# Kernel tuning notes

Measured on AMD Instinct MI355X. Metric: run time of the kernel, lower is better.

Reference implementation:

```python
import jax, jax.numpy as jnp
import numpy as np


def setup_inputs() -> dict:
    key = jax.random.key(0)
    kq, kv, ks = jax.random.split(key, 3)
    B, T, nh, N, D = 4, 2048, 8, 64, 128
    Q = jax.random.normal(kq, (B, T, nh, N), dtype=jnp.float32)
    V = jax.random.normal(kv, (B, T, D), dtype=jnp.float32)
    state = jax.random.normal(ks, (B, nh, N, D), dtype=jnp.float32)
    return {"Q": Q, "V": V, "state": state, "return_new_state": 1}


def reference(Q, V, state, return_new_state):
    # Inter-chunk: read recurrent state.  Q:[B,T,nh,N] x state:[B,nh,N,D] -> [B,T,nh,D]
    output = jnp.einsum('BTnN,BnND->BTnD', Q, state)
    new_state = None
    if return_new_state:
        # Q.flatten(2).mT @ V, unflattened: outer-product accumulation Q^T V
        new_state = state + jnp.einsum('BTnN,BTD->BnND', Q, V)
    T = Q.shape[1]
    if T > 1:
        # Strictly-causal intra-chunk term: tril(QQ^T, -1) @ V
        scores = jnp.tril(jnp.einsum('BTnN,BUnN->BnTU', Q, Q), k=-1)
        output = output + jnp.einsum('BnTU,BUD->BTnD', scores, V)
    return (output, new_state)
```

## Files before the change

### kernel.cpp

```cpp
#include <hip/hip_runtime.h>


using floatx4 = __attribute__((ext_vector_type(4))) float;
using float4v = __attribute__((ext_vector_type(4))) float;
using shortx8 = __attribute__((ext_vector_type(8))) short;
using shortx4 = __attribute__((ext_vector_type(4))) short;
using uint2v  = __attribute__((ext_vector_type(2))) unsigned int;

#define MFMA16(a, b, c) __builtin_amdgcn_mfma_f32_16x16x32_bf16((a), (b), (c), 0, 0, 0)

__device__ __forceinline__ unsigned short f2bf(float f) {
  unsigned int u = __builtin_bit_cast(unsigned int, f);
  u += 0x7FFFu + ((u >> 16) & 1u);
  return (unsigned short)(u >> 16);
}
__device__ __forceinline__ float bf2f(unsigned short h) {
  unsigned int u = ((unsigned int)h) << 16;
  return __builtin_bit_cast(float, u);
}
__device__ __forceinline__ unsigned int pack2(float a, float b) {
  return (unsigned int)f2bf(a) | ((unsigned int)f2bf(b) << 16);
}
__device__ __forceinline__ shortx8 lds8(const unsigned short* p) {
  shortx4 a = *(const shortx4*)p;
  shortx4 b = *(const shortx4*)(p + 4);
  return __builtin_shufflevector(a, b, 0, 1, 2, 3, 4, 5, 6, 7);
}

__global__ __launch_bounds__(256) void k_phase1(const float* __restrict__ Q,
                                                const float* __restrict__ V,
                                                float* __restrict__ ws1) {
  __shared__ unsigned short Qt[64 * 132];
  __shared__ unsigned short Vt[128 * 132];

  const int id = blockIdx.x;
  const int n = id >> 6, bg = id & 63, b = bg >> 4, g = bg & 15;
  const int t0 = g * 128;
  const int tid = threadIdx.x;

  const float* qbase = Q + (((size_t)(b * 2048 + t0) * 8 + n) * 64);
  const float* vbase = V + ((size_t)(b * 2048 + t0) * 128);

#pragma unroll 8
  for (int it = 0; it < 16; ++it) {
    int j = tid + it * 256;
    int i = j & 63, p = j >> 6;
    float q0 = qbase[(2 * p) * 512 + i];
    float q1 = qbase[(2 * p + 1) * 512 + i];
    *(unsigned int*)&Qt[i * 132 + 2 * p] = pack2(q0, q1);
  }
#pragma unroll 8
  for (int it = 0; it < 32; ++it) {
    int j = tid + it * 256;
    int d = j & 127, p = j >> 7;
    float v0 = vbase[(2 * p) * 128 + d];
    float v1 = vbase[(2 * p + 1) * 128 + d];
    *(unsigned int*)&Vt[d * 132 + 2 * p] = pack2(v0, v1);
  }
  __syncthreads();

  const int wave = tid >> 6, lane = tid & 63;
  const int col = lane & 15, quad = lane >> 4;

  floatx4 acc[4][2];
#pragma unroll
  for (int ti = 0; ti < 4; ++ti)
#pragma unroll
    for (int dj = 0; dj < 2; ++dj) acc[ti][dj] = (floatx4){0.f, 0.f, 0.f, 0.f};

#pragma unroll
  for (int s = 0; s < 4; ++s) {
    const int koff = s * 32 + quad * 8;
    shortx8 bv[2];
#pragma unroll
    for (int dj = 0; dj < 2; ++dj)
      bv[dj] = lds8(&Vt[((wave * 2 + dj) * 16 + col) * 132 + koff]);
#pragma unroll
    for (int ti = 0; ti < 4; ++ti) {
      shortx8 aq = lds8(&Qt[(ti * 16 + col) * 132 + koff]);
#pragma unroll
      for (int dj = 0; dj < 2; ++dj) acc[ti][dj] = MFMA16(aq, bv[dj], acc[ti][dj]);
    }
  }

  float* wbase = ws1 + (size_t)((b * 8 + n) * 16 + g) * 8192;
#pragma unroll
  for (int ti = 0; ti < 4; ++ti)
#pragma unroll
    for (int dj = 0; dj < 2; ++dj)
#pragma unroll
      for (int r = 0; r < 4; ++r) {
        int i = ti * 16 + quad * 4 + r;
        int d = (wave * 2 + dj) * 16 + col;
        wbase[i * 128 + d] = acc[ti][dj][r];
      }
}

__global__ __launch_bounds__(256) void k_prefix(const float* __restrict__ state,
                                                const float* __restrict__ ws1,
                                                unsigned short* __restrict__ ws2,
                                                float* __restrict__ new_state) {
  int t = blockIdx.x * 256 + threadIdx.x;
  int bn = t >> 13;
  int e = t & 8191;
  float run = state[bn * 8192 + e];
  const float* w1 = ws1 + (size_t)bn * 131072 + e;
  unsigned short* w2 = ws2 + (size_t)bn * 131072 + e;
#pragma unroll
  for (int g = 0; g < 16; ++g) {
    w2[g * 8192] = f2bf(run);
    run += w1[g * 8192];
  }
  new_state[bn * 8192 + e] = run;
}

__global__ __launch_bounds__(256) void k_phase2(const float* __restrict__ Q,
                                                const float* __restrict__ V,
                                                const unsigned short* __restrict__ ws2,
                                                float* __restrict__ out) {
  __shared__ unsigned short Qs[64 * 72];
  __shared__ unsigned short Vt[128 * 68];
  __shared__ unsigned short Ss[64 * 72];
  __shared__ unsigned short Pt[128 * 68];

  const int id = blockIdx.x;
  const int n = id >> 6, bg = id & 63, b = bg >> 4, g = bg & 15;
  const int t0 = g * 128;
  const int tid = threadIdx.x;
  const int wave = tid >> 6, lane = tid & 63;
  const int col = lane & 15, quad = lane >> 4;

  {
    const unsigned int* pb32 =
        (const unsigned int*)(ws2 + (size_t)((b * 8 + n) * 16 + g) * 8192);
#pragma unroll 8
    for (int it = 0; it < 16; ++it) {
      int j = tid + it * 256;
      int d2 = j & 63, i = j >> 6;
      unsigned int u = pb32[i * 64 + d2];
      Pt[(2 * d2) * 68 + i] = (unsigned short)(u & 0xFFFFu);
      Pt[(2 * d2 + 1) * 68 + i] = (unsigned short)(u >> 16);
    }
  }

  const float* qbase = Q + (((size_t)(b * 2048 + t0) * 8 + n) * 64);
  const float* vbase = V + ((size_t)(b * 2048 + t0) * 128);
  float* obase = out + (((size_t)(b * 2048 + t0) * 8 + n) * 128);

  for (int c = 0; c < 2; ++c) {
#pragma unroll
    for (int it = 0; it < 4; ++it) {
      int l = tid + it * 256;
      int t = l >> 4, k4 = (l & 15) * 4;
      float4v q = *(const float4v*)(qbase + (size_t)(c * 64 + t) * 512 + k4);
      uint2v u;
      u.x = pack2(q.x, q.y);
      u.y = pack2(q.z, q.w);
      *(uint2v*)&Qs[t * 72 + k4] = u;
    }
#pragma unroll 8
    for (int it = 0; it < 16; ++it) {
      int j = tid + it * 256;
      int d = j & 127, p = j >> 7;
      float v0 = vbase[(size_t)(c * 64 + 2 * p) * 128 + d];
      float v1 = vbase[(size_t)(c * 64 + 2 * p + 1) * 128 + d];
      *(unsigned int*)&Vt[d * 68 + 2 * p] = pack2(v0, v1);
    }
    __syncthreads();

    {
      int job = 0;
      for (int ti = 0; ti < 4; ++ti)
        for (int ui = 0; ui <= (ti | 1); ++ui, ++job) {
          if ((job & 3) != wave) continue;
          if (ui > ti) {
#pragma unroll
            for (int r = 0; r < 4; ++r)
              Ss[(ti * 16 + quad * 4 + r) * 72 + ui * 16 + col] = 0;
          } else {
            floatx4 sc = (floatx4){0.f, 0.f, 0.f, 0.f};
#pragma unroll
            for (int s = 0; s < 2; ++s) {
              shortx8 at = *(const shortx8*)&Qs[(ti * 16 + col) * 72 + s * 32 + quad * 8];
              shortx8 au = *(const shortx8*)&Qs[(ui * 16 + col) * 72 + s * 32 + quad * 8];
              sc = MFMA16(at, au, sc);
            }
#pragma unroll
            for (int r = 0; r < 4; ++r) {
              int t = ti * 16 + quad * 4 + r, u = ui * 16 + col;
              Ss[t * 72 + u] = (u < t) ? f2bf(sc[r]) : (unsigned short)0;
            }
          }
        }
    }
    __syncthreads();

    floatx4 acc[4][2];
#pragma unroll
    for (int ti = 0; ti < 4; ++ti)
#pragma unroll
      for (int dj = 0; dj < 2; ++dj) acc[ti][dj] = (floatx4){0.f, 0.f, 0.f, 0.f};

#pragma unroll
    for (int s = 0; s < 2; ++s) {
      const int koff = s * 32 + quad * 8;
      shortx8 bp[2];
#pragma unroll
      for (int dj = 0; dj < 2; ++dj)
        bp[dj] = lds8(&Pt[((wave * 2 + dj) * 16 + col) * 68 + koff]);
#pragma unroll
      for (int ti = 0; ti < 4; ++ti) {
        shortx8 aq = *(const shortx8*)&Qs[(ti * 16 + col) * 72 + koff];
#pragma unroll
        for (int dj = 0; dj < 2; ++dj) acc[ti][dj] = MFMA16(aq, bp[dj], acc[ti][dj]);
      }
    }
#pragma unroll
    for (int s = 0; s < 2; ++s) {
      const int koff = s * 32 + quad * 8;
      shortx8 bv[2];
#pragma unroll
      for (int dj = 0; dj < 2; ++dj)
        bv[dj] = lds8(&Vt[((wave * 2 + dj) * 16 + col) * 68 + koff]);
      for (int ti = (s == 0 ? 0 : 2); ti < 4; ++ti) {
        shortx8 as = *(const shortx8*)&Ss[(ti * 16 + col) * 72 + koff];
#pragma unroll
        for (int dj = 0; dj < 2; ++dj) acc[ti][dj] = MFMA16(as, bv[dj], acc[ti][dj]);
      }
    }
#pragma unroll
    for (int ti = 0; ti < 4; ++ti)
#pragma unroll
      for (int dj = 0; dj < 2; ++dj)
#pragma unroll
        for (int r = 0; r < 4; ++r) {
          int t = c * 64 + ti * 16 + quad * 4 + r;
          int d = (wave * 2 + dj) * 16 + col;
          obase[(size_t)t * 1024 + d] = acc[ti][dj][r];
        }

    if (c == 0) {
      floatx4 ua[8];
#pragma unroll
      for (int dm = 0; dm < 8; ++dm) ua[dm] = (floatx4){0.f, 0.f, 0.f, 0.f};
#pragma unroll
      for (int s = 0; s < 2; ++s) {
        const int koff = s * 32 + quad * 8;
        shortx8 bq;
#pragma unroll
        for (int jj = 0; jj < 8; ++jj)
          bq[jj] = (short)Qs[(koff + jj) * 72 + wave * 16 + col];
#pragma unroll
        for (int dm = 0; dm < 8; ++dm) {
          shortx8 av = lds8(&Vt[(dm * 16 + col) * 68 + koff]);
          ua[dm] = MFMA16(av, bq, ua[dm]);
        }
      }
      __syncthreads();
#pragma unroll
      for (int dm = 0; dm < 8; ++dm)
#pragma unroll
        for (int r = 0; r < 4; ++r) {
          int d = dm * 16 + quad * 4 + r;
          int i = wave * 16 + col;
          int idx = d * 68 + i;
          Pt[idx] = f2bf(bf2f(Pt[idx]) + ua[dm][r]);
        }
      __syncthreads();
    }
  }
}

extern "C" void kernel_launch(void* const* d_in, const int* in_sizes, int n_in,
                              void* d_out, int out_size, void* d_ws, size_t ws_size,
                              hipStream_t stream) {
  (void)in_sizes; (void)n_in; (void)out_size; (void)ws_size;
  const float* Q     = (const float*)d_in[0];
  const float* V     = (const float*)d_in[1];
  const float* state = (const float*)d_in[2];
  float* out        = (float*)d_out;
  float* new_state  = out + (size_t)4 * 2048 * 8 * 128;
  float* ws1        = (float*)d_ws;
  unsigned short* ws2 = (unsigned short*)((char*)d_ws + (size_t)512 * 8192 * 4);

  k_phase1<<<512, 256, 0, stream>>>(Q, V, ws1);
  k_prefix<<<1024, 256, 0, stream>>>(state, ws1, ws2, new_state);
  k_phase2<<<512, 256, 0, stream>>>(Q, V, ws2, out);
}
```

Measured before the change: 101.3 us.

## Shrink chunks to 64 tokens, store per-chunk partial states in bf16, reorder blocks

Halves the chunk size from 128 to 64 tokens, so phase1 and phase2 launch 1024 blocks and phase2 no longer carries a second sub-chunk with an in-block state update. Per-chunk partial states in the workspace become bf16 instead of fp32. The prefix kernel now scans 32 chunks, processing two elements per thread with paired bf16 loads and stores. Block ids are remapped so neighbouring blocks share batch and chunk. The changes aim to cut workspace traffic and serial work per block and to raise occupancy, at the cost of a longer prefix scan and extra bf16 rounding in the accumulated state.

```diff
diff --git a/kernel.cpp b/kernel.cpp
--- a/kernel.cpp
+++ b/kernel.cpp
@@ -3,6 +3,7 @@
 
 using floatx4 = __attribute__((ext_vector_type(4))) float;
 using float4v = __attribute__((ext_vector_type(4))) float;
+using float2v = __attribute__((ext_vector_type(2))) float;
 using shortx8 = __attribute__((ext_vector_type(8))) short;
 using shortx4 = __attribute__((ext_vector_type(4))) short;
 using uint2v  = __attribute__((ext_vector_type(2))) unsigned int;
@@ -27,35 +28,38 @@
   return __builtin_shufflevector(a, b, 0, 1, 2, 3, 4, 5, 6, 7);
 }
 
+#define DECODE_BNC()                                    \
+  const int id = blockIdx.x;                            \
+  const int n = (id >> 3) & 7;                          \
+  const int bc = (id >> 6) * 8 + (id & 7);              \
+  const int b = bc >> 5, c = bc & 31
+
 __global__ __launch_bounds__(256) void k_phase1(const float* __restrict__ Q,
                                                 const float* __restrict__ V,
-                                                float* __restrict__ ws1) {
-  __shared__ unsigned short Qt[64 * 132];
-  __shared__ unsigned short Vt[128 * 132];
-
-  const int id = blockIdx.x;
-  const int n = id >> 6, bg = id & 63, b = bg >> 4, g = bg & 15;
-  const int t0 = g * 128;
+                                                unsigned short* __restrict__ ws1) {
+  __shared__ unsigned short Qt[64 * 68];
+  __shared__ unsigned short Vt[128 * 68];
+
+  DECODE_BNC();
   const int tid = threadIdx.x;
-
-  const float* qbase = Q + (((size_t)(b * 2048 + t0) * 8 + n) * 64);
-  const float* vbase = V + ((size_t)(b * 2048 + t0) * 128);
-
-#pragma unroll 8
-  for (int it = 0; it < 16; ++it) {
+  const float* qbase = Q + (((size_t)(b * 2048 + c * 64) * 8 + n) * 64);
+  const float* vbase = V + ((size_t)(b * 2048 + c * 64) * 128);
+
+#pragma unroll
+  for (int it = 0; it < 8; ++it) {
     int j = tid + it * 256;
     int i = j & 63, p = j >> 6;
     float q0 = qbase[(2 * p) * 512 + i];
     float q1 = qbase[(2 * p + 1) * 512 + i];
-    *(unsigned int*)&Qt[i * 132 + 2 * p] = pack2(q0, q1);
-  }
-#pragma unroll 8
-  for (int it = 0; it < 32; ++it) {
+    *(unsigned int*)&Qt[i * 68 + 2 * p] = pack2(q0, q1);
+  }
+#pragma unroll
+  for (int it = 0; it < 16; ++it) {
     int j = tid + it * 256;
     int d = j & 127, p = j >> 7;
     float v0 = vbase[(2 * p) * 128 + d];
     float v1 = vbase[(2 * p + 1) * 128 + d];
-    *(unsigned int*)&Vt[d * 132 + 2 * p] = pack2(v0, v1);
+    *(unsigned int*)&Vt[d * 68 + 2 * p] = pack2(v0, v1);
   }
   __syncthreads();
 
@@ -69,21 +73,21 @@
     for (int dj = 0; dj < 2; ++dj) acc[ti][dj] = (floatx4){0.f, 0.f, 0.f, 0.f};
 
 #pragma unroll
-  for (int s = 0; s < 4; ++s) {
+  for (int s = 0; s < 2; ++s) {
     const int koff = s * 32 + quad * 8;
     shortx8 bv[2];
 #pragma unroll
     for (int dj = 0; dj < 2; ++dj)
-      bv[dj] = lds8(&Vt[((wave * 2 + dj) * 16 + col) * 132 + koff]);
+      bv[dj] = lds8(&Vt[((wave * 2 + dj) * 16 + col) * 68 + koff]);
 #pragma unroll
     for (int ti = 0; ti < 4; ++ti) {
-      shortx8 aq = lds8(&Qt[(ti * 16 + col) * 132 + koff]);
+      shortx8 aq = lds8(&Qt[(ti * 16 + col) * 68 + koff]);
 #pragma unroll
       for (int dj = 0; dj < 2; ++dj) acc[ti][dj] = MFMA16(aq, bv[dj], acc[ti][dj]);
     }
   }
 
-  float* wbase = ws1 + (size_t)((b * 8 + n) * 16 + g) * 8192;
+  unsigned short* wbase = ws1 + (size_t)((b * 8 + n) * 32 + c) * 8192;
 #pragma unroll
   for (int ti = 0; ti < 4; ++ti)
 #pragma unroll
@@ -92,26 +96,30 @@
       for (int r = 0; r < 4; ++r) {
         int i = ti * 16 + quad * 4 + r;
         int d = (wave * 2 + dj) * 16 + col;
-        wbase[i * 128 + d] = acc[ti][dj][r];
+        wbase[i * 128 + d] = f2bf(acc[ti][dj][r]);
       }
 }
 
 __global__ __launch_bounds__(256) void k_prefix(const float* __restrict__ state,
-                                                const float* __restrict__ ws1,
-                                                unsigned short* __restrict__ ws2,
+                                                const unsigned int* __restrict__ ws1,
+                                                unsigned int* __restrict__ ws2,
                                                 float* __restrict__ new_state) {
   int t = blockIdx.x * 256 + threadIdx.x;
-  int bn = t >> 13;
-  int e = t & 8191;
-  float run = state[bn * 8192 + e];
-  const float* w1 = ws1 + (size_t)bn * 131072 + e;
-  unsigned short* w2 = ws2 + (size_t)bn * 131072 + e;
-#pragma unroll
-  for (int g = 0; g < 16; ++g) {
-    w2[g * 8192] = f2bf(run);
-    run += w1[g * 8192];
-  }
-  new_state[bn * 8192 + e] = run;
+  int bn = t >> 12;
+  int e2 = t & 4095;
+  float2v st = *(const float2v*)(state + (size_t)bn * 8192 + 2 * e2);
+  float run0 = st.x, run1 = st.y;
+  const unsigned int* w1 = ws1 + (size_t)bn * 32 * 4096 + e2;
+  unsigned int* w2 = ws2 + (size_t)bn * 32 * 4096 + e2;
+#pragma unroll
+  for (int g = 0; g < 32; ++g) {
+    w2[g * 4096] = pack2(run0, run1);
+    unsigned int s = w1[g * 4096];
+    run0 += bf2f((unsigned short)(s & 0xFFFFu));
+    run1 += bf2f((unsigned short)(s >> 16));
+  }
+  float2v ns; ns.x = run0; ns.y = run1;
+  *(float2v*)(new_state + (size_t)bn * 8192 + 2 * e2) = ns;
 }
 
 __global__ __launch_bounds__(256) void k_phase2(const float* __restrict__ Q,
@@ -123,17 +131,15 @@
   __shared__ unsigned short Ss[64 * 72];
   __shared__ unsigned short Pt[128 * 68];
 
-  const int id = blockIdx.x;
-  const int n = id >> 6, bg = id & 63, b = bg >> 4, g = bg & 15;
-  const int t0 = g * 128;
+  DECODE_BNC();
   const int tid = threadIdx.x;
   const int wave = tid >> 6, lane = tid & 63;
   const int col = lane & 15, quad = lane >> 4;
 
   {
     const unsigned int* pb32 =
-        (const unsigned int*)(ws2 + (size_t)((b * 8 + n) * 16 + g) * 8192);
-#pragma unroll 8
+        (const unsigned int*)(ws2 + (size_t)((b * 8 + n) * 32 + c) * 8192);
+#pragma unroll
     for (int it = 0; it < 16; ++it) {
       int j = tid + it * 256;
       int d2 = j & 63, i = j >> 6;
@@ -143,132 +149,100 @@
     }
   }
 
-  const float* qbase = Q + (((size_t)(b * 2048 + t0) * 8 + n) * 64);
-  const float* vbase = V + ((size_t)(b * 2048 + t0) * 128);
-  float* obase = out + (((size_t)(b * 2048 + t0) * 8 + n) * 128);
-
-  for (int c = 0; c < 2; ++c) {
-#pragma unroll
-    for (int it = 0; it < 4; ++it) {
-      int l = tid + it * 256;
-      int t = l >> 4, k4 = (l & 15) * 4;
-      float4v q = *(const float4v*)(qbase + (size_t)(c * 64 + t) * 512 + k4);
-      uint2v u;
-      u.x = pack2(q.x, q.y);
-      u.y = pack2(q.z, q.w);
-      *(uint2v*)&Qs[t * 72 + k4] = u;
-    }
-#pragma unroll 8
-    for (int it = 0; it < 16; ++it) {
-      int j = tid + it * 256;
-      int d = j & 127, p = j >> 7;
-      float v0 = vbase[(size_t)(c * 64 + 2 * p) * 128 + d];
-      float v1 = vbase[(size_t)(c * 64 + 2 * p + 1) * 128 + d];
-      *(unsigned int*)&Vt[d * 68 + 2 * p] = pack2(v0, v1);
-    }
-    __syncthreads();
-
-    {
-      int job = 0;
-      for (int ti = 0; ti < 4; ++ti)
-        for (int ui = 0; ui <= (ti | 1); ++ui, ++job) {
-          if ((job & 3) != wave) continue;
-          if (ui > ti) {
-#pragma unroll
-            for (int r = 0; r < 4; ++r)
-              Ss[(ti * 16 + quad * 4 + r) * 72 + ui * 16 + col] = 0;
-          } else {
-            floatx4 sc = (floatx4){0.f, 0.f, 0.f, 0.f};
-#pragma unroll
-            for (int s = 0; s < 2; ++s) {
-              shortx8 at = *(const shortx8*)&Qs[(ti * 16 + col) * 72 + s * 32 + quad * 8];
-              shortx8 au = *(const shortx8*)&Qs[(ui * 16 + col) * 72 + s * 32 + quad * 8];
-              sc = MFMA16(at, au, sc);
-            }
-#pragma unroll
-            for (int r = 0; r < 4; ++r) {
-              int t = ti * 16 + quad * 4 + r, u = ui * 16 + col;
-              Ss[t * 72 + u] = (u < t) ? f2bf(sc[r]) : (unsigned short)0;
-            }
+  const float* qbase = Q + (((size_t)(b * 2048 + c * 64) * 8 + n) * 64);
+  const float* vbase = V + ((size_t)(b * 2048 + c * 64) * 128);
+  float* obase = out + (((size_t)(b * 2048 + c * 64) * 8 + n) * 128);
+
+#pragma unroll
+  for (int it = 0; it < 4; ++it) {
+    int l = tid + it * 256;
+    int t = l >> 4, k4 = (l & 15) * 4;
+    float4v q = *(const float4v*)(qbase + (size_t)t * 512 + k4);
+    uint2v u;
+    u.x = pack2(q.x, q.y);
+    u.y = pack2(q.z, q.w);
+    *(uint2v*)&Qs[t * 72 + k4] = u;
+  }
+#pragma unroll
+  for (int it = 0; it < 16; ++it) {
+    int j = tid + it * 256;
+    int d = j & 127, p = j >> 7;
+    float v0 = vbase[(size_t)(2 * p) * 128 + d];
+    float v1 = vbase[(size_t)(2 * p + 1) * 128 + d];
+    *(unsigned int*)&Vt[d * 68 + 2 * p] = pack2(v0, v1);
+  }
+  __syncthreads();
+
+  {
+    int job = 0;
+    for (int ti = 0; ti < 4; ++ti)
+      for (int ui = 0; ui <= (ti | 1); ++ui, ++job) {
+        if ((job & 3) != wave) continue;
+        if (ui > ti) {
+#pragma unroll
+          for (int r = 0; r < 4; ++r)
+            Ss[(ti * 16 + quad * 4 + r) * 72 + ui * 16 + col] = 0;
+        } else {
+          floatx4 sc = (floatx4){0.f, 0.f, 0.f, 0.f};
+#pragma unroll
+          for (int s = 0; s < 2; ++s) {
+            shortx8 at = *(const shortx8*)&Qs[(ti * 16 + col) * 72 + s * 32 + quad * 8];
+            shortx8 au = *(const shortx8*)&Qs[(ui * 16 + col) * 72 + s * 32 + quad * 8];
+            sc = MFMA16(at, au, sc);
+          }
+#pragma unroll
+          for (int r = 0; r < 4; ++r) {
+            int t = ti * 16 + quad * 4 + r, u = ui * 16 + col;
+            Ss[t * 72 + u] = (u < t) ? f2bf(sc[r]) : (unsigned short)0;
           }
         }
-    }
-    __syncthreads();
-
-    floatx4 acc[4][2];
-#pragma unroll
-    for (int ti = 0; ti < 4; ++ti)
-#pragma unroll
-      for (int dj = 0; dj < 2; ++dj) acc[ti][dj] = (floatx4){0.f, 0.f, 0.f, 0.f};
-
-#pragma unroll
-    for (int s = 0; s < 2; ++s) {
-      const int koff = s * 32 + quad * 8;
-      shortx8 bp[2];
-#pragma unroll
-      for (int dj = 0; dj < 2; ++dj)
-        bp[dj] = lds8(&Pt[((wave * 2 + dj) * 16 + col) * 68 + koff]);
-#pragma unroll
-      for (int ti = 0; ti < 4; ++ti) {
-        shortx8 aq = *(const shortx8*)&Qs[(ti * 16 + col) * 72 + koff];
-#pragma unroll
-        for (int dj = 0; dj < 2; ++dj) acc[ti][dj] = MFMA16(aq, bp[dj], acc[ti][dj]);
       }
-    }
-#pragma unroll
-    for (int s = 0; s < 2; ++s) {
-      const int koff = s * 32 + quad * 8;
-      shortx8 bv[2];
-#pragma unroll
-      for (int dj = 0; dj < 2; ++dj)
-        bv[dj] = lds8(&Vt[((wave * 2 + dj) * 16 + col) * 68 + koff]);
-      for (int ti = (s == 0 ? 0 : 2); ti < 4; ++ti) {
-        shortx8 as = *(const shortx8*)&Ss[(ti * 16 + col) * 72 + koff];
-#pragma unroll
-        for (int dj = 0; dj < 2; ++dj) acc[ti][dj] = MFMA16(as, bv[dj], acc[ti][dj]);
+  }
+  __syncthreads();
+
+  floatx4 acc[4][2];
+#pragma unroll
+  for (int ti = 0; ti < 4; ++ti)
+#pragma unroll
+    for (int dj = 0; dj < 2; ++dj) acc[ti][dj] = (floatx4){0.f, 0.f, 0.f, 0.f};
+
+#pragma unroll
+  for (int s = 0; s < 2; ++s) {
+    const int koff = s * 32 + quad * 8;
+    shortx8 bp[2];
+#pragma unroll
+    for (int dj = 0; dj < 2; ++dj)
+      bp[dj] = lds8(&Pt[((wave * 2 + dj) * 16 + col) * 68 + koff]);
+#pragma unroll
+    for (int ti = 0; ti < 4; ++ti) {
+      shortx8 aq = *(const shortx8*)&Qs[(ti * 16 + col) * 72 + koff];
+#pragma unroll
+      for (int dj = 0; dj < 2; ++dj) acc[ti][dj] = MFMA16(aq, bp[dj], acc[ti][dj]);
+    }
+  }
+#pragma unroll
+  for (int s = 0; s < 2; ++s) {
+    const int koff = s * 32 + quad * 8;
+    shortx8 bv[2];
+#pragma unroll
+    for (int dj = 0; dj < 2; ++dj)
+      bv[dj] = lds8(&Vt[((wave * 2 + dj) * 16 + col) * 68 + koff]);
+    for (int ti = (s == 0 ? 0 : 2); ti < 4; ++ti) {
+      shortx8 as = *(const shortx8*)&Ss[(ti * 16 + col) * 72 + koff];
+#pragma unroll
+      for (int dj = 0; dj < 2; ++dj) acc[ti][dj] = MFMA16(as, bv[dj], acc[ti][dj]);
+    }
+  }
+#pragma unroll
+  for (int ti = 0; ti < 4; ++ti)
+#pragma unroll
+    for (int dj = 0; dj < 2; ++dj)
+#pragma unroll
+      for (int r = 0; r < 4; ++r) {
+        int t = ti * 16 + quad * 4 + r;
+        int d = (wave * 2 + dj) * 16 + col;
+        obase[(size_t)t * 1024 + d] = acc[ti][dj][r];
       }
-    }
-#pragma unroll
-    for (int ti = 0; ti < 4; ++ti)
-#pragma unroll
-      for (int dj = 0; dj < 2; ++dj)
-#pragma unroll
-        for (int r = 0; r < 4; ++r) {
-          int t = c * 64 + ti * 16 + quad * 4 + r;
-          int d = (wave * 2 + dj) * 16 + col;
-          obase[(size_t)t * 1024 + d] = acc[ti][dj][r];
-        }
-
-    if (c == 0) {
-      floatx4 ua[8];
-#pragma unroll
-      for (int dm = 0; dm < 8; ++dm) ua[dm] = (floatx4){0.f, 0.f, 0.f, 0.f};
-#pragma unroll
-      for (int s = 0; s < 2; ++s) {
-        const int koff = s * 32 + quad * 8;
-        shortx8 bq;
-#pragma unroll
-        for (int jj = 0; jj < 8; ++jj)
-          bq[jj] = (short)Qs[(koff + jj) * 72 + wave * 16 + col];
-#pragma unroll
-        for (int dm = 0; dm < 8; ++dm) {
-          shortx8 av = lds8(&Vt[(dm * 16 + col) * 68 + koff]);
-          ua[dm] = MFMA16(av, bq, ua[dm]);
-        }
-      }
-      __syncthreads();
-#pragma unroll
-      for (int dm = 0; dm < 8; ++dm)
-#pragma unroll
-        for (int r = 0; r < 4; ++r) {
-          int d = dm * 16 + quad * 4 + r;
-          int i = wave * 16 + col;
-          int idx = d * 68 + i;
-          Pt[idx] = f2bf(bf2f(Pt[idx]) + ua[dm][r]);
-        }
-      __syncthreads();
-    }
-  }
 }
 
 extern "C" void kernel_launch(void* const* d_in, const int* in_sizes, int n_in,
@@ -280,10 +254,11 @@
   const float* state = (const float*)d_in[2];
   float* out        = (float*)d_out;
   float* new_state  = out + (size_t)4 * 2048 * 8 * 128;
-  float* ws1        = (float*)d_ws;
-  unsigned short* ws2 = (unsigned short*)((char*)d_ws + (size_t)512 * 8192 * 4);
-
-  k_phase1<<<512, 256, 0, stream>>>(Q, V, ws1);
-  k_prefix<<<1024, 256, 0, stream>>>(state, ws1, ws2, new_state);
-  k_phase2<<<512, 256, 0, stream>>>(Q, V, ws2, out);
-}
+  unsigned short* ws1 = (unsigned short*)d_ws;
+  unsigned short* ws2 = ws1 + (size_t)32 * 32 * 8192;
+
+  k_phase1<<<1024, 256, 0, stream>>>(Q, V, ws1);
+  k_prefix<<<512, 256, 0, stream>>>(state, (const unsigned int*)ws1,
+                                    (unsigned int*)ws2, new_state);
+  k_phase2<<<1024, 256, 0, stream>>>(Q, V, ws2, out);
+}
```

Result: slower. 104.6 us (+3.2%).
